# Kernel tuning notes

Measured on AMD Instinct MI355X. Metric: run time of the kernel, lower is better.

The kernel has to match this reference:

```python
import jax, jax.numpy as jnp
import numpy as np

T = 0.04
PIC_NUM = 4  # images per identity (hardcoded in SP_loss)


def setup_inputs() -> dict:
    key = jax.random.key(0)
    N, D = 8192, 256  # 2048 identities x 4 images, 256-dim ReID features
    x = jax.random.normal(key, (N, D), dtype=jnp.float32)
    x = x / jnp.linalg.norm(x, axis=1, keepdims=True)  # L2-normalize (cosine sims)
    return {"x": x}


def reference(x):
    N = x.shape[0]
    G = N // PIC_NUM  # number of identity groups
    s = (x @ x.T) / T  # [N, N] scaled similarity matrix

    # Diagonal 4x4 blocks: within-class similarities. [G, 4, 4]
    d4 = s.reshape(G, PIC_NUM, G, PIC_NUM)
    gidx = jnp.arange(G)
    pos = d4[gidx, :, gidx, :]  # [G, 4, 4]

    # hard positive: -T * log( sum_{i,j in class} exp(-dot_ij / T) )  (soft-min)
    hard_pos = -T * jax.nn.logsumexp(-pos.reshape(G, PIC_NUM * PIC_NUM), axis=1)

    # least-hard positive: T * log( sum_i 1 / (sum_j exp(-dot_ij / T)) )
    lse_row = jax.nn.logsumexp(-pos, axis=2)           # [G, 4] = log sum_j exp(-dot/T)
    least_pos = T * jax.nn.logsumexp(-lse_row, axis=1)  # [G]

    # negatives: T * log( sum_{i in class, j not in class} exp(dot_ij / T) )
    col_group = jnp.arange(N) // PIC_NUM              # [N]
    same = col_group[None, :] == gidx[:, None]        # [G, N] same-class column mask
    s3 = s.reshape(G, PIC_NUM, N)
    neg_masked = jnp.where(same[:, None, :], -jnp.inf, s3)
    neg = T * jax.nn.logsumexp(neg_masked.reshape(G, PIC_NUM * N), axis=1)  # [G]

    # Original detaches all three S vectors before forming the loss.
    hard_pos = jax.lax.stop_gradient(hard_pos)
    least_pos = jax.lax.stop_gradient(least_pos)
    neg = jax.lax.stop_gradient(neg)

    # alpha: harmonic mean of (hard, least-hard) when hard >= 0, else 0
    alpha = jnp.where(hard_pos >= 0.0,
                      2.0 * least_pos * hard_pos / (hard_pos + least_pos),
                      0.0)
    margin = alpha * hard_pos + (1.0 - alpha) * least_pos
    # log(1 + exp(z)) == softplus(z), numerically stable, same math
    loss = jnp.mean(jax.nn.softplus((neg - margin) / T))
    return loss
```

## Files before the change

### kernel.cpp

```cpp
#include <hip/hip_runtime.h>
#include <hip/hip_bf16.h>
#include <math.h>


#define NROWS 8192
#define DDIM  256
#define NGRP  2048
#define T_CONST 0.04f
#define INV_T   25.0f

typedef __attribute__((ext_vector_type(8))) short bf16x8_t;
typedef __attribute__((ext_vector_type(4))) float f32x4_t;

typedef const __attribute__((address_space(1))) void gv_t;
typedef __attribute__((address_space(3))) void lv_t;

__device__ __forceinline__ unsigned short f2bf_rne(float f) {
    unsigned int u = __float_as_uint(f);
    unsigned int r = 0x7fffu + ((u >> 16) & 1u);
    return (unsigned short)((u + r) >> 16);
}

__device__ __forceinline__ void gll16(const unsigned short* g, unsigned short* l) {
    __builtin_amdgcn_global_load_lds((gv_t*)g, (lv_t*)l, 16, 0, 0);
}

__global__ __launch_bounds__(256) void cvt_zero_kernel(const float* __restrict__ x,
                                                       unsigned short* __restrict__ xb,
                                                       float* __restrict__ rowsum) {
    int gid = blockIdx.x * 256 + threadIdx.x;
    int i = gid * 4;
    float4 v = *(const float4*)(x + i);
    ushort4 b;
    b.x = f2bf_rne(v.x); b.y = f2bf_rne(v.y); b.z = f2bf_rne(v.z); b.w = f2bf_rne(v.w);
    *(ushort4*)(xb + i) = b;
    if (gid < NROWS) rowsum[gid] = 0.f;
}

__global__ __launch_bounds__(64) void pos_margin_kernel(const float* __restrict__ x,
                                                        float* __restrict__ margin) {
    const int g = blockIdx.x;
    const int lane = threadIdx.x;
    const float* xr = x + (size_t)g * 4 * DDIM;
    float a[16];
#pragma unroll
    for (int k = 0; k < 16; ++k) a[k] = 0.f;
    for (int e = lane; e < DDIM; e += 64) {
        float vv[4];
        vv[0] = xr[e];
        vv[1] = xr[DDIM + e];
        vv[2] = xr[2 * DDIM + e];
        vv[3] = xr[3 * DDIM + e];
#pragma unroll
        for (int i = 0; i < 4; ++i)
#pragma unroll
            for (int j = 0; j < 4; ++j)
                a[i * 4 + j] = fmaf(vv[i], vv[j], a[i * 4 + j]);
    }
#pragma unroll
    for (int k = 0; k < 16; ++k) {
        float t = a[k];
        t += __shfl_xor(t, 32, 64);
        t += __shfl_xor(t, 16, 64);
        t += __shfl_xor(t, 8, 64);
        t += __shfl_xor(t, 4, 64);
        t += __shfl_xor(t, 2, 64);
        t += __shfl_xor(t, 1, 64);
        a[k] = t;
    }
    if (lane == 0) {
        float pos[16];
#pragma unroll
        for (int k = 0; k < 16; ++k) pos[k] = a[k] * INV_T;

        float mx = -pos[0];
#pragma unroll
        for (int k = 1; k < 16; ++k) mx = fmaxf(mx, -pos[k]);
        float se = 0.f;
#pragma unroll
        for (int k = 0; k < 16; ++k) se += __expf(-pos[k] - mx);
        float hard_pos = -T_CONST * (mx + __logf(se));

        float lse_row[4];
#pragma unroll
        for (int i = 0; i < 4; ++i) {
            float m2 = -pos[i * 4];
#pragma unroll
            for (int j = 1; j < 4; ++j) m2 = fmaxf(m2, -pos[i * 4 + j]);
            float s2 = 0.f;
#pragma unroll
            for (int j = 0; j < 4; ++j) s2 += __expf(-pos[i * 4 + j] - m2);
            lse_row[i] = m2 + __logf(s2);
        }
        float m3 = -lse_row[0];
#pragma unroll
        for (int i = 1; i < 4; ++i) m3 = fmaxf(m3, -lse_row[i]);
        float s3 = 0.f;
#pragma unroll
        for (int i = 0; i < 4; ++i) s3 += __expf(-lse_row[i] - m3);
        float least_pos = T_CONST * (m3 + __logf(s3));

        float alpha = (hard_pos >= 0.f)
                          ? (2.f * least_pos * hard_pos) / (hard_pos + least_pos)
                          : 0.f;
        margin[g] = alpha * hard_pos + (1.f - alpha) * least_pos;
    }
}

__global__ __launch_bounds__(256) void gemm_exp_rowsum(const unsigned short* __restrict__ xb,
                                                       float* __restrict__ rowsum) {
    __shared__ unsigned short Als[128 * 32];
    __shared__ unsigned short Bls[128 * 32];
    __shared__ float rowacc[128];

    const int tid = threadIdx.x;
    const int lane = tid & 63;
    const int w = tid >> 6;
    const int row0 = blockIdx.y * 128;
    const int col0 = blockIdx.x * 128;
    const int wrow = (w >> 1) * 64;
    const int wcol = (w & 1) * 64;
    const int quad = lane >> 4;
    const int l16 = lane & 15;
    const int srow = tid >> 2;
    const int scol = (tid & 3) * 8;

    if (tid < 128) rowacc[tid] = 0.f;

    f32x4_t acc[4][4];
#pragma unroll
    for (int i = 0; i < 4; ++i)
#pragma unroll
        for (int j = 0; j < 4; ++j)
            acc[i][j] = (f32x4_t){0.f, 0.f, 0.f, 0.f};

    const unsigned short* ga = xb + (size_t)(row0 + srow) * DDIM + scol;
    const unsigned short* gb = xb + (size_t)(col0 + srow) * DDIM + scol;

    for (int kb = 0; kb < DDIM; kb += 32) {
        if (kb) __syncthreads();
        gll16(ga + kb,              &Als[tid * 8]);
        gll16(ga + kb + 64 * DDIM,  &Als[2048 + tid * 8]);
        gll16(gb + kb,              &Bls[tid * 8]);
        gll16(gb + kb + 64 * DDIM,  &Bls[2048 + tid * 8]);
        __syncthreads();

        bf16x8_t aF[4], bF[4];
#pragma unroll
        for (int mi = 0; mi < 4; ++mi)
            aF[mi] = *(const bf16x8_t*)&Als[(wrow + mi * 16 + l16) * 32 + quad * 8];
#pragma unroll
        for (int ni = 0; ni < 4; ++ni)
            bF[ni] = *(const bf16x8_t*)&Bls[(wcol + ni * 16 + l16) * 32 + quad * 8];
#pragma unroll
        for (int mi = 0; mi < 4; ++mi)
#pragma unroll
            for (int ni = 0; ni < 4; ++ni)
                acc[mi][ni] = __builtin_amdgcn_mfma_f32_16x16x32_bf16(aF[mi], bF[ni],
                                                                      acc[mi][ni], 0, 0, 0);
    }

#pragma unroll
    for (int mi = 0; mi < 4; ++mi) {
#pragma unroll
        for (int reg = 0; reg < 4; ++reg) {
            const int lrow = wrow + mi * 16 + quad * 4 + reg;
            const int grp = (row0 + lrow) >> 2;
            float v = 0.f;
#pragma unroll
            for (int ni = 0; ni < 4; ++ni) {
                const int gcol = col0 + wcol + ni * 16 + l16;
                const float sv = acc[mi][ni][reg] * INV_T;
                v += ((gcol >> 2) == grp) ? 0.f : __expf(sv);
            }
            v += __shfl_xor(v, 1, 64);
            v += __shfl_xor(v, 2, 64);
            v += __shfl_xor(v, 4, 64);
            v += __shfl_xor(v, 8, 64);
            if (l16 == 0) atomicAdd(&rowacc[lrow], v);
        }
    }
    __syncthreads();
    if (tid < 128) atomicAdd(&rowsum[row0 + tid], rowacc[tid]);
}

__global__ __launch_bounds__(256) void finalize_kernel(const float* __restrict__ rowsum,
                                                       const float* __restrict__ margin,
                                                       float* __restrict__ out) {
    const int tid = threadIdx.x;
    float local = 0.f;
    for (int g = tid; g < NGRP; g += 256) {
        float s = rowsum[4 * g] + rowsum[4 * g + 1] + rowsum[4 * g + 2] + rowsum[4 * g + 3];
        float z = __logf(s) - margin[g] * INV_T;
        float sp = (z > 30.f) ? z : log1pf(__expf(z));
        local += sp;
    }
    local += __shfl_xor(local, 1, 64);
    local += __shfl_xor(local, 2, 64);
    local += __shfl_xor(local, 4, 64);
    local += __shfl_xor(local, 8, 64);
    local += __shfl_xor(local, 16, 64);
    local += __shfl_xor(local, 32, 64);
    __shared__ float wsum[4];
    if ((tid & 63) == 0) wsum[tid >> 6] = local;
    __syncthreads();
    if (tid == 0) out[0] = (wsum[0] + wsum[1] + wsum[2] + wsum[3]) * (1.f / (float)NGRP);
}

extern "C" void kernel_launch(void* const* d_in, const int* in_sizes, int n_in,
                              void* d_out, int out_size, void* d_ws, size_t ws_size,
                              hipStream_t stream) {
    const float* x = (const float*)d_in[0];
    float* out = (float*)d_out;

    unsigned short* xb = (unsigned short*)d_ws;
    float* rowsum = (float*)((char*)d_ws + (size_t)NROWS * DDIM * 2);
    float* margin = rowsum + NROWS;

    cvt_zero_kernel<<<(NROWS * DDIM / 4) / 256, 256, 0, stream>>>(x, xb, rowsum);
    pos_margin_kernel<<<NGRP, 64, 0, stream>>>(x, margin);
    gemm_exp_rowsum<<<dim3(64, 64), 256, 0, stream>>>(xb, rowsum);
    finalize_kernel<<<1, 256, 0, stream>>>(rowsum, margin, out);
}
```

Baseline: 126.4 us.

## Exploit symmetry of similarity matrix with triangular tiles, swizzle LDS, fuse prep kernels

The GEMM now launches only the upper-triangular 128x128 tiles of the symmetric x·xᵀ matrix. Each off-diagonal tile adds its exp sums to both the row sums and the transposed column sums, which roughly halves the MFMA and exp work. A swizzled LDS layout (XOR of the k-chunk index) is added to cut bank conflicts on fragment reads. The conversion and positive-margin kernels are merged into one launch. The cost is extra column reductions and global atomics per tile, plus a sqrt-based decode of the tile index.

```diff
diff --git a/kernel.cpp b/kernel.cpp
--- a/kernel.cpp
+++ b/kernel.cpp
@@ -6,6 +6,7 @@
 #define NROWS 8192
 #define DDIM  256
 #define NGRP  2048
+#define NTB   64
 #define T_CONST 0.04f
 #define INV_T   25.0f
 
@@ -25,22 +26,23 @@
     __builtin_amdgcn_global_load_lds((gv_t*)g, (lv_t*)l, 16, 0, 0);
 }
 
-__global__ __launch_bounds__(256) void cvt_zero_kernel(const float* __restrict__ x,
-                                                       unsigned short* __restrict__ xb,
-                                                       float* __restrict__ rowsum) {
-    int gid = blockIdx.x * 256 + threadIdx.x;
-    int i = gid * 4;
-    float4 v = *(const float4*)(x + i);
-    ushort4 b;
-    b.x = f2bf_rne(v.x); b.y = f2bf_rne(v.y); b.z = f2bf_rne(v.z); b.w = f2bf_rne(v.w);
-    *(ushort4*)(xb + i) = b;
-    if (gid < NROWS) rowsum[gid] = 0.f;
-}
-
-__global__ __launch_bounds__(64) void pos_margin_kernel(const float* __restrict__ x,
-                                                        float* __restrict__ margin) {
-    const int g = blockIdx.x;
-    const int lane = threadIdx.x;
+__global__ __launch_bounds__(256) void prep_kernel(const float* __restrict__ x,
+                                                   unsigned short* __restrict__ xb,
+                                                   float* __restrict__ rowsum,
+                                                   float* __restrict__ margin) {
+    const int b = blockIdx.x;
+    if (b < 2048) {
+        int gid = b * 256 + threadIdx.x;
+        int i = gid * 4;
+        float4 v = *(const float4*)(x + i);
+        ushort4 o;
+        o.x = f2bf_rne(v.x); o.y = f2bf_rne(v.y); o.z = f2bf_rne(v.z); o.w = f2bf_rne(v.w);
+        *(ushort4*)(xb + i) = o;
+        if (gid < NROWS) rowsum[gid] = 0.f;
+        return;
+    }
+    const int g = (b - 2048) * 4 + (threadIdx.x >> 6);
+    const int lane = threadIdx.x & 63;
     const float* xr = x + (size_t)g * 4 * DDIM;
     float a[16];
 #pragma unroll
@@ -112,20 +114,29 @@
     __shared__ unsigned short Als[128 * 32];
     __shared__ unsigned short Bls[128 * 32];
     __shared__ float rowacc[128];
+    __shared__ float colacc[128];
+
+    const int idx = blockIdx.x;
+    int bi = (int)((129.0f - sqrtf(16641.0f - 8.0f * (float)idx)) * 0.5f);
+    while (bi * (129 - bi) / 2 > idx) --bi;
+    while ((bi + 1) * (128 - bi) / 2 <= idx) ++bi;
+    const int bj = bi + (idx - bi * (129 - bi) / 2);
+    const int row0 = bi * 128;
+    const int col0 = bj * 128;
+    const bool diag = (bi == bj);
 
     const int tid = threadIdx.x;
     const int lane = tid & 63;
     const int w = tid >> 6;
-    const int row0 = blockIdx.y * 128;
-    const int col0 = blockIdx.x * 128;
     const int wrow = (w >> 1) * 64;
     const int wcol = (w & 1) * 64;
     const int quad = lane >> 4;
     const int l16 = lane & 15;
+    const int swz = (l16 >> 1) & 3;
     const int srow = tid >> 2;
-    const int scol = (tid & 3) * 8;
-
-    if (tid < 128) rowacc[tid] = 0.f;
+    const int kc = (tid & 3) ^ ((tid >> 3) & 3);
+
+    if (tid < 128) { rowacc[tid] = 0.f; colacc[tid] = 0.f; }
 
     f32x4_t acc[4][4];
 #pragma unroll
@@ -134,24 +145,24 @@
         for (int j = 0; j < 4; ++j)
             acc[i][j] = (f32x4_t){0.f, 0.f, 0.f, 0.f};
 
-    const unsigned short* ga = xb + (size_t)(row0 + srow) * DDIM + scol;
-    const unsigned short* gb = xb + (size_t)(col0 + srow) * DDIM + scol;
+    const unsigned short* ga = xb + (size_t)(row0 + srow) * DDIM + kc * 8;
+    const unsigned short* gb = xb + (size_t)(col0 + srow) * DDIM + kc * 8;
 
     for (int kb = 0; kb < DDIM; kb += 32) {
         if (kb) __syncthreads();
-        gll16(ga + kb,              &Als[tid * 8]);
-        gll16(ga + kb + 64 * DDIM,  &Als[2048 + tid * 8]);
-        gll16(gb + kb,              &Bls[tid * 8]);
-        gll16(gb + kb + 64 * DDIM,  &Bls[2048 + tid * 8]);
+        gll16(ga + kb,             &Als[tid * 8]);
+        gll16(ga + kb + 64 * DDIM, &Als[2048 + tid * 8]);
+        gll16(gb + kb,             &Bls[tid * 8]);
+        gll16(gb + kb + 64 * DDIM, &Bls[2048 + tid * 8]);
         __syncthreads();
 
         bf16x8_t aF[4], bF[4];
 #pragma unroll
         for (int mi = 0; mi < 4; ++mi)
-            aF[mi] = *(const bf16x8_t*)&Als[(wrow + mi * 16 + l16) * 32 + quad * 8];
+            aF[mi] = *(const bf16x8_t*)&Als[(wrow + mi * 16 + l16) * 32 + (quad ^ swz) * 8];
 #pragma unroll
         for (int ni = 0; ni < 4; ++ni)
-            bF[ni] = *(const bf16x8_t*)&Bls[(wcol + ni * 16 + l16) * 32 + quad * 8];
+            bF[ni] = *(const bf16x8_t*)&Bls[(wcol + ni * 16 + l16) * 32 + (quad ^ swz) * 8];
 #pragma unroll
         for (int mi = 0; mi < 4; ++mi)
 #pragma unroll
@@ -160,28 +171,60 @@
                                                                       acc[mi][ni], 0, 0, 0);
     }
 
-#pragma unroll
-    for (int mi = 0; mi < 4; ++mi) {
-#pragma unroll
-        for (int reg = 0; reg < 4; ++reg) {
-            const int lrow = wrow + mi * 16 + quad * 4 + reg;
-            const int grp = (row0 + lrow) >> 2;
-            float v = 0.f;
-#pragma unroll
-            for (int ni = 0; ni < 4; ++ni) {
-                const int gcol = col0 + wcol + ni * 16 + l16;
-                const float sv = acc[mi][ni][reg] * INV_T;
-                v += ((gcol >> 2) == grp) ? 0.f : __expf(sv);
+    if (!diag) {
+        float colv[4] = {0.f, 0.f, 0.f, 0.f};
+#pragma unroll
+        for (int mi = 0; mi < 4; ++mi) {
+#pragma unroll
+            for (int reg = 0; reg < 4; ++reg) {
+                const int lrow = wrow + mi * 16 + quad * 4 + reg;
+                float rv = 0.f;
+#pragma unroll
+                for (int ni = 0; ni < 4; ++ni) {
+                    float e = __expf(acc[mi][ni][reg] * INV_T);
+                    rv += e;
+                    colv[ni] += e;
+                }
+                rv += __shfl_xor(rv, 1, 64);
+                rv += __shfl_xor(rv, 2, 64);
+                rv += __shfl_xor(rv, 4, 64);
+                rv += __shfl_xor(rv, 8, 64);
+                if (l16 == 0) atomicAdd(&rowacc[lrow], rv);
             }
-            v += __shfl_xor(v, 1, 64);
-            v += __shfl_xor(v, 2, 64);
-            v += __shfl_xor(v, 4, 64);
-            v += __shfl_xor(v, 8, 64);
-            if (l16 == 0) atomicAdd(&rowacc[lrow], v);
+        }
+#pragma unroll
+        for (int ni = 0; ni < 4; ++ni) {
+            float cv = colv[ni];
+            cv += __shfl_xor(cv, 16, 64);
+            cv += __shfl_xor(cv, 32, 64);
+            if (quad == 0) atomicAdd(&colacc[wcol + ni * 16 + l16], cv);
+        }
+    } else {
+#pragma unroll
+        for (int mi = 0; mi < 4; ++mi) {
+#pragma unroll
+            for (int reg = 0; reg < 4; ++reg) {
+                const int lrow = wrow + mi * 16 + quad * 4 + reg;
+                const int grp = (row0 + lrow) >> 2;
+                float rv = 0.f;
+#pragma unroll
+                for (int ni = 0; ni < 4; ++ni) {
+                    const int gcol = col0 + wcol + ni * 16 + l16;
+                    rv += ((gcol >> 2) == grp) ? 0.f : __expf(acc[mi][ni][reg] * INV_T);
+                }
+                rv += __shfl_xor(rv, 1, 64);
+                rv += __shfl_xor(rv, 2, 64);
+                rv += __shfl_xor(rv, 4, 64);
+                rv += __shfl_xor(rv, 8, 64);
+                if (l16 == 0) atomicAdd(&rowacc[lrow], rv);
+            }
         }
     }
     __syncthreads();
-    if (tid < 128) atomicAdd(&rowsum[row0 + tid], rowacc[tid]);
+    if (tid < 128) {
+        atomicAdd(&rowsum[row0 + tid], rowacc[tid]);
+        if (!diag) atomicAdd(&rowsum[col0 + tid], colacc[tid]);
+    }
 }
 
 __global__ __launch_bounds__(256) void finalize_kernel(const float* __restrict__ rowsum,
@@ -217,8 +260,7 @@
     float* rowsum = (float*)((char*)d_ws + (size_t)NROWS * DDIM * 2);
     float* margin = rowsum + NROWS;
 
-    cvt_zero_kernel<<<(NROWS * DDIM / 4) / 256, 256, 0, stream>>>(x, xb, rowsum);
-    pos_margin_kernel<<<NGRP, 64, 0, stream>>>(x, margin);
-    gemm_exp_rowsum<<<dim3(64, 64), 256, 0, stream>>>(xb, rowsum);
+    prep_kernel<<<2048 + 512, 256, 0, stream>>>(x, xb, rowsum, margin);
+    gemm_exp_rowsum<<<NTB * (NTB + 1) / 2, 256, 0, stream>>>(xb, rowsum);
     finalize_kernel<<<1, 256, 0, stream>>>(rowsum, margin, out);
 }
```

New measurement: 116.5 us. 1.09x faster.
